# Optimization experiments

Measured on AMD Instinct MI355X. Metric: run time of the kernel, lower is better.

## Reference

```python
import jax, jax.numpy as jnp
import numpy as np

N_NODES = 50000
EPS = 1e-5


def setup_inputs() -> dict:
    key = jax.random.key(0)
    ks = jax.random.split(key, 8)
    B, N, F, H = 2, N_NODES, 128, 128
    E = 800000
    x = jax.random.normal(ks[0], (B, N, F), dtype=jnp.float32)
    edge_index = jax.random.randint(ks[1], (2, E), 0, N, dtype=jnp.int32)
    # Xavier-uniform weights, zero biases (matches reset_parameters)
    def xavier(k, fin, fout):
        lim = np.sqrt(6.0 / (fin + fout)).astype(np.float32)
        return jax.random.uniform(k, (fin, fout), jnp.float32, -lim, lim)
    return {
        "x": x,
        "edge_index": edge_index,
        "W1": xavier(ks[2], F, H), "b1": jnp.zeros((H,), jnp.float32),
        "W2": xavier(ks[3], H, H), "b2": jnp.zeros((H,), jnp.float32),
        "W3": xavier(ks[4], H, 1), "b3": jnp.zeros((1,), jnp.float32),
        "gamma1": jnp.ones((H,), jnp.float32), "beta1": jnp.zeros((H,), jnp.float32),
        "gamma2": jnp.ones((H,), jnp.float32), "beta2": jnp.zeros((H,), jnp.float32),
    }


def _gconv(h, edge_index, W, b):
    # h: [B, N, Fin] -> support: [B, N, Fout]
    sup = jnp.einsum('bnf,fo->bno', h, W)
    row, col = edge_index[0], edge_index[1]
    # gather source rows, scatter-add into destination rows (per batch, vmapped)
    agg = jax.vmap(lambda s: jax.ops.segment_sum(s[row], col, num_segments=N_NODES))(sup)
    return agg + b


def _bn(h, gamma, beta):
    # BatchNorm1d over flattened (B*N, F): training-mode batch statistics
    m = jnp.mean(h, axis=(0, 1))
    v = jnp.var(h, axis=(0, 1))
    return (h - m) * jax.lax.rsqrt(v + EPS) * gamma + beta


def reference(x, edge_index, W1, b1, W2, b2, W3, b3, gamma1, beta1, gamma2, beta2):
    h = _gconv(x, edge_index, W1, b1)
    h = jax.nn.relu(_bn(h, gamma1, beta1))
    h = _gconv(h, edge_index, W2, b2)
    h = jax.nn.relu(_bn(h, gamma2, beta2))
    out = _gconv(h, edge_index, W3, b3)
    return out[..., 0]  # squeeze(-1) -> [B, N]
```

## Files before the change

### kernel.cpp

```cpp
#include <hip/hip_runtime.h>

#define N_NODES 50000
#define N_EDGES 800000
#define NROWS 100000
#define BN_EPS 1e-5f
#define CAP 64
#define NREP 64

typedef unsigned short ushort_t;
typedef unsigned int uint_t;
typedef __attribute__((ext_vector_type(8))) short bf16x8;
typedef __attribute__((ext_vector_type(4))) float f32x4;

__device__ inline ushort_t f2bf(float f) {
    uint_t x = __float_as_uint(f);
    x += 0x7fffu + ((x >> 16) & 1u);
    return (ushort_t)(x >> 16);
}
__device__ inline float4 bf4_to_f4(ushort4 u) {
    float4 f;
    f.x = __uint_as_float((uint_t)u.x << 16);
    f.y = __uint_as_float((uint_t)u.y << 16);
    f.z = __uint_as_float((uint_t)u.z << 16);
    f.w = __uint_as_float((uint_t)u.w << 16);
    return f;
}
__device__ inline void round4(float4 v, bf16x8& hi, int base) {
    hi[base + 0] = (short)f2bf(v.x);
    hi[base + 1] = (short)f2bf(v.y);
    hi[base + 2] = (short)f2bf(v.z);
    hi[base + 3] = (short)f2bf(v.w);
}

__global__ __launch_bounds__(256) void k_init(const float* __restrict__ W1,
                                              const float* __restrict__ W2,
                                              ushort_t* __restrict__ wt,
                                              int* __restrict__ cnt,
                                              float* __restrict__ stats) {
    int idx = blockIdx.x * 256 + threadIdx.x;
    for (int i = idx; i < N_NODES; i += 32768) cnt[i] = 0;
    stats[idx] = 0.f;
    int which = idx >> 14;
    int e = idx & 16383;
    int k = e >> 7, n = e & 127;
    float f = (which ? W2 : W1)[e];
    ushort_t h = f2bf(f);
    float fh = __uint_as_float((uint_t)h << 16);
    ushort_t l = f2bf(f - fh);
    size_t base = (size_t)which * 32768;
    wt[base + n * 128 + k] = h;
    wt[base + 16384 + n * 128 + k] = l;
}

template <bool BN>
__device__ __forceinline__ void gemm_tile(int tile,
                                          const float* __restrict__ A,
                                          const ushort_t* __restrict__ wt,
                                          const float* __restrict__ stats,
                                          const float* __restrict__ gamma,
                                          const float* __restrict__ beta,
                                          ushort_t* __restrict__ C,
                                          short* lds, float* cs, int tid) {
    long r0 = (long)tile * 64;
    const float4* A4 = (const float4*)A;

    if (BN) {
        if (tid < 128) {
            float s = 0.f, s2 = 0.f;
            for (int r = 0; r < NREP; ++r) {
                s  += stats[r * 256 + tid];
                s2 += stats[r * 256 + 128 + tid];
            }
            float inv = 1.0f / (float)NROWS;
            float mean = s * inv;
            float var = s2 * inv - mean * mean;
            float scale = gamma[tid] / sqrtf(var + BN_EPS);
            cs[tid] = scale;
            cs[128 + tid] = beta[tid] - mean * scale;
        }
        __syncthreads();
    }
    const float4* coef4 = (const float4*)cs;

    #pragma unroll
    for (int i = 0; i < 4; ++i) {
        int li = tid + i * 256;
        int r = li >> 4, j = li & 15;
        long gr = r0 + r;
        float4 va = make_float4(0.f, 0.f, 0.f, 0.f), vb = va;
        if (gr < NROWS) { va = A4[gr * 32 + j * 2]; vb = A4[gr * 32 + j * 2 + 1]; }
        if (BN) {
            float4 sc = coef4[j * 2], sh = coef4[32 + j * 2];
            va.x = fmaxf(va.x * sc.x + sh.x, 0.f);
            va.y = fmaxf(va.y * sc.y + sh.y, 0.f);
            va.z = fmaxf(va.z * sc.z + sh.z, 0.f);
            va.w = fmaxf(va.w * sc.w + sh.w, 0.f);
            sc = coef4[j * 2 + 1]; sh = coef4[32 + j * 2 + 1];
            vb.x = fmaxf(vb.x * sc.x + sh.x, 0.f);
            vb.y = fmaxf(vb.y * sc.y + sh.y, 0.f);
            vb.z = fmaxf(vb.z * sc.z + sh.z, 0.f);
            vb.w = fmaxf(vb.w * sc.w + sh.w, 0.f);
        }
        bf16x8 vh;
        round4(va, vh, 0);
        round4(vb, vh, 4);
        *(bf16x8*)&lds[r * 128 + ((j ^ (r & 15)) * 8)] = vh;
    }

    int w = tid >> 6, l = tid & 63;
    int m = l & 15, q = l >> 4;
    for (int half = 0; half < 2; ++half) {
        __syncthreads();
        #pragma unroll
        for (int i = 0; i < 8; ++i) {
            int li = tid + i * 256;
            int p = li >> 10;
            int rest = li & 1023;
            int nl = rest >> 4, j = rest & 15;
            bf16x8 v = *(const bf16x8*)&wt[(size_t)p * 16384 + (half * 64 + nl) * 128 + j * 8];
            *(bf16x8*)&lds[8192 + p * 8192 + nl * 128 + ((j ^ (nl & 15)) * 8)] = v;
        }
        __syncthreads();

        f32x4 acc[4] = {};
        #pragma unroll
        for (int s = 0; s < 4; ++s) {
            int x = (s * 4 + q) ^ m;
            bf16x8 ah = *(const bf16x8*)&lds[(w * 16 + m) * 128 + x * 8];
            #pragma unroll
            for (int c = 0; c < 4; ++c) {
                int boff = 8192 + (c * 16 + m) * 128 + x * 8;
                bf16x8 bh = *(const bf16x8*)&lds[boff];
                bf16x8 bl = *(const bf16x8*)&lds[8192 + boff];
                acc[c] = __builtin_amdgcn_mfma_f32_16x16x32_bf16(ah, bl, acc[c], 0, 0, 0);
                acc[c] = __builtin_amdgcn_mfma_f32_16x16x32_bf16(ah, bh, acc[c], 0, 0, 0);
            }
        }

        #pragma unroll
        for (int c = 0; c < 4; ++c) {
            #pragma unroll
            for (int r = 0; r < 4; ++r) {
                long gr = r0 + w * 16 + q * 4 + r;
                if (gr < NROWS) {
                    int b = gr >= N_NODES;
                    long node = gr - (long)b * N_NODES;
                    C[(node * 2 + b) * 128 + half * 64 + c * 16 + m] = f2bf(acc[c][r]);
                }
            }
        }
    }
}

__global__ __launch_bounds__(256) void k_work(const float* __restrict__ x,
                                              const int* __restrict__ rowp,
                                              const int* __restrict__ colp,
                                              const ushort_t* __restrict__ wt,
                                              int* __restrict__ cnt,
                                              ushort_t* __restrict__ srcbuf,
                                              ushort_t* __restrict__ sup) {
    __shared__ short lds[24576];
    __shared__ float cs[256];
    int b = blockIdx.x;
    int q = b / 3, r3 = b - q * 3;
    if (r3 == 0) {
        gemm_tile<false>(q, x, wt, nullptr, nullptr, nullptr, sup, lds, cs, threadIdx.x);
    } else {
        int cid = q * 2 + (r3 - 1);
        int e = cid * 256 + threadIdx.x;
        int c = colp[e];
        int p = atomicAdd(&cnt[c], 1);
        if (p < CAP) srcbuf[(c << 6) + p] = (ushort_t)rowp[e];
    }
}

__global__ __launch_bounds__(256) void k_gemm_bn(const float* __restrict__ A,
                                                 const ushort_t* __restrict__ wt,
                                                 const float* __restrict__ stats,
                                                 const float* __restrict__ gamma,
                                                 const float* __restrict__ beta,
                                                 ushort_t* __restrict__ C) {
    __shared__ short lds[24576];
    __shared__ float cs[256];
    gemm_tile<true>(blockIdx.x, A, wt, stats, gamma, beta, C, lds, cs, threadIdx.x);
}

__global__ __launch_bounds__(256) void aggregate_bf16(const ushort_t* __restrict__ sup,
                                                      const int* __restrict__ cnt,
                                                      const ushort_t* __restrict__ srcbuf,
                                                      float* __restrict__ agg,
                                                      float* __restrict__ stats) {
    __shared__ float lsb[4][256];
    int lane = threadIdx.x & 63;
    int wid = threadIdx.x >> 6;
    int node = blockIdx.x * 4 + wid;
    int s = lane >> 5;
    int l32 = lane & 31;
    int m = cnt[node]; if (m > CAP) m = CAP;
    const ushort4* sb = (const ushort4*)sup;
    float4 a0 = make_float4(0.f, 0.f, 0.f, 0.f);
    float4 a1 = make_float4(0.f, 0.f, 0.f, 0.f);
    int idx = (lane < m) ? (int)srcbuf[(node << 6) + lane] : 0;
    int tmax = (m + 1) >> 1;
    #pragma unroll 2
    for (int t = 0; t < tmax; ++t) {
        int j = 2 * t + s;
        int r = __shfl(idx, j & 63);
        ushort4 u0 = sb[(size_t)r * 64 + l32];
        ushort4 u1 = sb[(size_t)r * 64 + 32 + l32];
        if (j < m) {
            float4 f0 = bf4_to_f4(u0);
            float4 f1 = bf4_to_f4(u1);
            a0.x += f0.x; a0.y += f0.y; a0.z += f0.z; a0.w += f0.w;
            a1.x += f1.x; a1.y += f1.y; a1.z += f1.z; a1.w += f1.w;
        }
    }
    a0.x += __shfl_xor(a0.x, 32); a0.y += __shfl_xor(a0.y, 32);
    a0.z += __shfl_xor(a0.z, 32); a0.w += __shfl_xor(a0.w, 32);
    a1.x += __shfl_xor(a1.x, 32); a1.y += __shfl_xor(a1.y, 32);
    a1.z += __shfl_xor(a1.z, 32); a1.w += __shfl_xor(a1.w, 32);
    float4* ag = (float4*)agg;
    if (s == 0) {
        ag[(size_t)node * 32 + l32] = a0;
        lsb[wid][l32 * 8 + 0] = a0.x + a1.x;
        lsb[wid][l32 * 8 + 1] = a0.y + a1.y;
        lsb[wid][l32 * 8 + 2] = a0.z + a1.z;
        lsb[wid][l32 * 8 + 3] = a0.w + a1.w;
        lsb[wid][l32 * 8 + 4] = a0.x * a0.x + a1.x * a1.x;
        lsb[wid][l32 * 8 + 5] = a0.y * a0.y + a1.y * a1.y;
        lsb[wid][l32 * 8 + 6] = a0.z * a0.z + a1.z * a1.z;
        lsb[wid][l32 * 8 + 7] = a0.w * a0.w + a1.w * a1.w;
    } else {
        ag[(size_t)(N_NODES + node) * 32 + l32] = a1;
    }
    __syncthreads();
    int tid = threadIdx.x;
    float v = lsb[0][tid] + lsb[1][tid] + lsb[2][tid] + lsb[3][tid];
    int f = (tid >> 3) * 4 + (tid & 3);
    int isq = (tid >> 2) & 1;
    atomicAdd(&stats[(blockIdx.x & (NREP - 1)) * 256 + isq * 128 + f], v);
}

__global__ __launch_bounds__(256) void gemv_bn_kernel(const float* __restrict__ h,
                                                      const float* __restrict__ stats,
                                                      const float* __restrict__ gamma,
                                                      const float* __restrict__ beta,
                                                      const float* __restrict__ W3,
                                                      float* __restrict__ sup3) {
    __shared__ float cs[256];
    int tid = threadIdx.x;
    if (tid < 128) {
        float s = 0.f, s2 = 0.f;
        for (int r = 0; r < NREP; ++r) {
            s  += stats[r * 256 + tid];
            s2 += stats[r * 256 + 128 + tid];
        }
        float inv = 1.0f / (float)NROWS;
        float mean = s * inv;
        float var = s2 * inv - mean * mean;
        float scale = gamma[tid] / sqrtf(var + BN_EPS);
        cs[tid] = scale;
        cs[128 + tid] = beta[tid] - mean * scale;
    }
    __syncthreads();
    int lane = tid & 63, wid = tid >> 6;
    float2 w  = ((const float2*)W3)[lane];
    float2 sc = ((const float2*)cs)[lane];
    float2 sh = ((const float2*)(cs + 128))[lane];
    #pragma unroll
    for (int r = 0; r < 4; ++r) {
        long gw = (long)blockIdx.x * 16 + wid * 4 + r;
        float2 v = ((const float2*)h)[(size_t)gw * 64 + lane];
        v.x = fmaxf(v.x * sc.x + sh.x, 0.f);
        v.y = fmaxf(v.y * sc.y + sh.y, 0.f);
        float s = v.x * w.x + v.y * w.y;
        #pragma unroll
        for (int d = 32; d > 0; d >>= 1) s += __shfl_xor(s, d);
        if (lane == 0) sup3[gw] = s;
    }
}

__global__ __launch_bounds__(256) void gather_out_kernel(const int* __restrict__ cnt,
                                                         const ushort_t* __restrict__ srcbuf,
                                                         const float* __restrict__ sup3,
                                                         const float* __restrict__ b3,
                                                         float* __restrict__ out) {
    int gtid = blockIdx.x * 256 + threadIdx.x;
    if (gtid >= 2 * N_NODES) return;
    int n = gtid >> 1, bb = gtid & 1;
    int m = cnt[n]; if (m > CAP) m = CAP;
    int base = n << 6;
    const float* s3 = sup3 + (size_t)bb * N_NODES;
    float s = 0.f;
    for (int i = 0; i < m; ++i) s += s3[srcbuf[base + i]];
    out[(size_t)bb * N_NODES + n] = s + b3[0];
}

extern "C" void kernel_launch(void* const* d_in, const int* in_sizes, int n_in,
                              void* d_out, int out_size, void* d_ws, size_t ws_size,
                              hipStream_t stream) {
    const float* x      = (const float*)d_in[0];
    const int*   ei     = (const int*)d_in[1];
    const float* W1     = (const float*)d_in[2];
    const float* W2     = (const float*)d_in[4];
    const float* W3     = (const float*)d_in[6];
    const float* b3     = (const float*)d_in[7];
    const float* gamma1 = (const float*)d_in[8];
    const float* beta1  = (const float*)d_in[9];
    const float* gamma2 = (const float*)d_in[10];
    const float* beta2  = (const float*)d_in[11];
    const int* rowp = ei;
    const int* colp = ei + N_EDGES;

    ushort_t* sup   = (ushort_t*)d_ws;
    float* agg      = (float*)(sup + 12800000);
    float* sup3     = agg + 12800000;
    ushort_t* wt    = (ushort_t*)(sup3 + 100000);
    float* stats    = (float*)(wt + 65536);
    int*   cnt      = (int*)(stats + 32768);
    ushort_t* srcbuf = (ushort_t*)(cnt + N_NODES);
    float* out      = (float*)d_out;
    float* stats2   = stats + 16384;

    k_init <<<128,  256, 0, stream>>>(W1, W2, wt, cnt, stats);
    k_work <<<4688, 256, 0, stream>>>(x, rowp, colp, wt, cnt, srcbuf, sup);

    aggregate_bf16 <<<12500, 256, 0, stream>>>(sup, cnt, srcbuf, agg, stats);
    k_gemm_bn      <<<1563,  256, 0, stream>>>(agg, wt + 32768, stats, gamma1, beta1, sup);
    aggregate_bf16 <<<12500, 256, 0, stream>>>(sup, cnt, srcbuf, agg, stats2);

    gemv_bn_kernel   <<<6250, 256, 0, stream>>>(agg, stats2, gamma2, beta2, W3, sup3);
    gather_out_kernel<<<391,  256, 0, stream>>>(cnt, srcbuf, sup3, b3, out);
}
```

Before: 337.3 us.

## Slice support features by XCD so random aggregation gathers stay L2-resident

The GEMM epilogue now writes the bf16 support matrix in eight 16-feature slices, each slice holding all nodes of both batches contiguously. The aggregation kernel is rewritten so each block handles 64 nodes for one slice, chosen as blockIdx&7. This appears intended to line up with round-robin XCD dispatch, so each XCD's L2 only has to hold one small slice during the random neighbor gathers. Each lane now gathers 16 bytes per edge with per-lane index loads and a wave-wide max trip count, and BN statistics are reduced with shuffles. The cost is less coalesced gathers and extra loop iterations for lanes with fewer neighbors.

```diff
diff --git a/kernel.cpp b/kernel.cpp
--- a/kernel.cpp
+++ b/kernel.cpp
@@ -16,14 +16,6 @@
     uint_t x = __float_as_uint(f);
     x += 0x7fffu + ((x >> 16) & 1u);
     return (ushort_t)(x >> 16);
-}
-__device__ inline float4 bf4_to_f4(ushort4 u) {
-    float4 f;
-    f.x = __uint_as_float((uint_t)u.x << 16);
-    f.y = __uint_as_float((uint_t)u.y << 16);
-    f.z = __uint_as_float((uint_t)u.z << 16);
-    f.w = __uint_as_float((uint_t)u.w << 16);
-    return f;
 }
 __device__ inline void round4(float4 v, bf16x8& hi, int base) {
     hi[base + 0] = (short)f2bf(v.x);
@@ -145,7 +137,8 @@
                 if (gr < NROWS) {
                     int b = gr >= N_NODES;
                     long node = gr - (long)b * N_NODES;
-                    C[(node * 2 + b) * 128 + half * 64 + c * 16 + m] = f2bf(acc[c][r]);
+                    C[((size_t)(half * 4 + c) * (N_NODES * 2) + node * 2 + b) * 16 + m] =
+                        f2bf(acc[c][r]);
                 }
             }
         }
@@ -190,55 +183,73 @@
                                                       const ushort_t* __restrict__ srcbuf,
                                                       float* __restrict__ agg,
                                                       float* __restrict__ stats) {
-    __shared__ float lsb[4][256];
-    int lane = threadIdx.x & 63;
-    int wid = threadIdx.x >> 6;
-    int node = blockIdx.x * 4 + wid;
-    int s = lane >> 5;
-    int l32 = lane & 31;
-    int m = cnt[node]; if (m > CAP) m = CAP;
-    const ushort4* sb = (const ushort4*)sup;
-    float4 a0 = make_float4(0.f, 0.f, 0.f, 0.f);
-    float4 a1 = make_float4(0.f, 0.f, 0.f, 0.f);
-    int idx = (lane < m) ? (int)srcbuf[(node << 6) + lane] : 0;
-    int tmax = (m + 1) >> 1;
+    __shared__ float lds_s[64], lds_q[64];
+    int tid = threadIdx.x;
+    int lane = tid & 63, w = tid >> 6;
+    int slice = blockIdx.x & 7;
+    int group = blockIdx.x >> 3;
+    int g = lane >> 2, j = lane & 3;
+    int b = j >> 1, fh = j & 1;
+    int node = group * 64 + w * 16 + g;
+    bool valid = node < N_NODES;
+    int nodec = valid ? node : 0;
+    int m = 0;
+    if (valid) { m = cnt[node]; if (m > CAP) m = CAP; }
+    int wm = m;
+    wm = max(wm, __shfl_xor(wm, 4));
+    wm = max(wm, __shfl_xor(wm, 8));
+    wm = max(wm, __shfl_xor(wm, 16));
+    wm = max(wm, __shfl_xor(wm, 32));
+
+    const ushort_t* sslice = sup + (size_t)slice * (2u * N_NODES * 16);
+    int boff = b * 16 + fh * 8;
+    size_t nbase = (size_t)nodec << 6;
+
+    float a[8] = {0.f, 0.f, 0.f, 0.f, 0.f, 0.f, 0.f, 0.f};
     #pragma unroll 2
-    for (int t = 0; t < tmax; ++t) {
-        int j = 2 * t + s;
-        int r = __shfl(idx, j & 63);
-        ushort4 u0 = sb[(size_t)r * 64 + l32];
-        ushort4 u1 = sb[(size_t)r * 64 + 32 + l32];
-        if (j < m) {
-            float4 f0 = bf4_to_f4(u0);
-            float4 f1 = bf4_to_f4(u1);
-            a0.x += f0.x; a0.y += f0.y; a0.z += f0.z; a0.w += f0.w;
-            a1.x += f1.x; a1.y += f1.y; a1.z += f1.z; a1.w += f1.w;
-        }
-    }
-    a0.x += __shfl_xor(a0.x, 32); a0.y += __shfl_xor(a0.y, 32);
-    a0.z += __shfl_xor(a0.z, 32); a0.w += __shfl_xor(a0.w, 32);
-    a1.x += __shfl_xor(a1.x, 32); a1.y += __shfl_xor(a1.y, 32);
-    a1.z += __shfl_xor(a1.z, 32); a1.w += __shfl_xor(a1.w, 32);
-    float4* ag = (float4*)agg;
-    if (s == 0) {
-        ag[(size_t)node * 32 + l32] = a0;
-        lsb[wid][l32 * 8 + 0] = a0.x + a1.x;
-        lsb[wid][l32 * 8 + 1] = a0.y + a1.y;
-        lsb[wid][l32 * 8 + 2] = a0.z + a1.z;
-        lsb[wid][l32 * 8 + 3] = a0.w + a1.w;
-        lsb[wid][l32 * 8 + 4] = a0.x * a0.x + a1.x * a1.x;
-        lsb[wid][l32 * 8 + 5] = a0.y * a0.y + a1.y * a1.y;
-        lsb[wid][l32 * 8 + 6] = a0.z * a0.z + a1.z * a1.z;
-        lsb[wid][l32 * 8 + 7] = a0.w * a0.w + a1.w * a1.w;
-    } else {
-        ag[(size_t)(N_NODES + node) * 32 + l32] = a1;
+    for (int t = 0; t < wm; ++t) {
+        int r = (int)__builtin_nontemporal_load(&srcbuf[nbase + t]);
+        if (t < m) {
+            const bf16x8 u = *(const bf16x8*)&sslice[(size_t)r * 32 + boff];
+            #pragma unroll
+            for (int k = 0; k < 8; ++k)
+                a[k] += __uint_as_float((uint_t)(ushort_t)u[k] << 16);
+        }
+    }
+
+    if (valid) {
+        float* ap = agg + ((size_t)b * N_NODES + node) * 128 + slice * 16 + fh * 8;
+        f32x4 v0 = {a[0], a[1], a[2], a[3]};
+        f32x4 v1 = {a[4], a[5], a[6], a[7]};
+        __builtin_nontemporal_store(v0, (f32x4*)ap);
+        __builtin_nontemporal_store(v1, (f32x4*)(ap + 4));
+    }
+
+    float qv[8];
+    #pragma unroll
+    for (int k = 0; k < 8; ++k) qv[k] = a[k] * a[k];
+    #pragma unroll
+    for (int d = 2; d <= 32; d <<= 1) {
+        #pragma unroll
+        for (int k = 0; k < 8; ++k) {
+            a[k]  += __shfl_xor(a[k], d);
+            qv[k] += __shfl_xor(qv[k], d);
+        }
+    }
+    if (lane < 2) {
+        #pragma unroll
+        for (int k = 0; k < 8; ++k) {
+            lds_s[w * 16 + lane * 8 + k] = a[k];
+            lds_q[w * 16 + lane * 8 + k] = qv[k];
+        }
     }
     __syncthreads();
-    int tid = threadIdx.x;
-    float v = lsb[0][tid] + lsb[1][tid] + lsb[2][tid] + lsb[3][tid];
-    int f = (tid >> 3) * 4 + (tid & 3);
-    int isq = (tid >> 2) & 1;
-    atomicAdd(&stats[(blockIdx.x & (NREP - 1)) * 256 + isq * 128 + f], v);
+    if (tid < 32) {
+        int which = tid >> 4, f = tid & 15;
+        const float* src = which ? lds_q : lds_s;
+        float v = src[f] + src[16 + f] + src[32 + f] + src[48 + f];
+        atomicAdd(&stats[(group & (NREP - 1)) * 256 + which * 128 + slice * 16 + f], v);
+    }
 }
 
 __global__ __launch_bounds__(256) void gemv_bn_kernel(const float* __restrict__ h,
@@ -325,9 +336,9 @@
     k_init <<<128,  256, 0, stream>>>(W1, W2, wt, cnt, stats);
     k_work <<<4688, 256, 0, stream>>>(x, rowp, colp, wt, cnt, srcbuf, sup);
 
-    aggregate_bf16 <<<12500, 256, 0, stream>>>(sup, cnt, srcbuf, agg, stats);
-    k_gemm_bn      <<<1563,  256, 0, stream>>>(agg, wt + 32768, stats, gamma1, beta1, sup);
-    aggregate_bf16 <<<12500, 256, 0, stream>>>(sup, cnt, srcbuf, agg, stats2);
+    aggregate_bf16 <<<6256, 256, 0, stream>>>(sup, cnt, srcbuf, agg, stats);
+    k_gemm_bn      <<<1563, 256, 0, stream>>>(agg, wt + 32768, stats, gamma1, beta1, sup);
+    aggregate_bf16 <<<6256, 256, 0, stream>>>(sup, cnt, srcbuf, agg, stats2);
 
     gemv_bn_kernel   <<<6250, 256, 0, stream>>>(agg, stats2, gamma2, beta2, W3, sup3);
     gather_out_kernel<<<391,  256, 0, stream>>>(cnt, srcbuf, sup3, b3, out);
```

Measured after the change: 576.3 us. 1.71x slower.
